# Optimization experiments

Measured on AMD Instinct MI355X. Metric: run time of the kernel, lower is better.

Reference implementation:

```python
import jax, jax.numpy as jnp
import numpy as np

B, S, H = 2, 1024, 4096
NH, DH, NKV = 32, 128, 2          # heads, head_dim, kv groups
ROT = DH // 2                      # 64: GLM rotates first half of head dim
GROUP = NH // NKV                  # 16 query heads per kv group
SCALE = DH ** -0.5


def glm_rope(x, pos):
    """GLM interleaved rotary on first ROT dims. x: [B,S,h,DH], pos: [B,S] int."""
    rot, rest = x[..., :ROT], x[..., ROT:]
    inv_freq = 1.0 / (10000.0 ** (jnp.arange(0, ROT, 2, dtype=jnp.float32) / ROT))  # [ROT/2]
    ang = pos.astype(jnp.float32)[:, :, None] * inv_freq[None, None, :]             # [B,S,ROT/2]
    cos = jnp.cos(ang)[:, :, None, :]
    sin = jnp.sin(ang)[:, :, None, :]
    x0, x1 = rot[..., 0::2], rot[..., 1::2]
    o0 = x0 * cos - x1 * sin
    o1 = x1 * cos + x0 * sin
    rot_out = jnp.stack([o0, o1], axis=-1).reshape(rot.shape)
    return jnp.concatenate([rot_out, rest], axis=-1)


def setup_inputs() -> dict:
    key = jax.random.key(0)
    k1, k2, k3, k4 = jax.random.split(key, 4)
    return {
        "hidden_states": jax.random.normal(k1, (B, S, H), jnp.float32) * 0.02,
        "position_ids": jnp.arange(B * S, dtype=jnp.int32).reshape(B, S) % S,
        "W_qkv": jax.random.normal(k2, (H, NH * DH + 2 * NKV * DH), jnp.float32) * 0.02,
        "b_qkv": jax.random.normal(k3, (NH * DH + 2 * NKV * DH,), jnp.float32) * 0.02,
        "W_dense": jax.random.normal(k4, (NH * DH, H), jnp.float32) * 0.02,
    }


def reference(hidden_states, position_ids, W_qkv, b_qkv, W_dense):
    qkv = hidden_states @ W_qkv + b_qkv                              # [B,S,4608]
    q = qkv[..., : NH * DH].reshape(B, S, NH, DH)
    k = qkv[..., NH * DH : NH * DH + NKV * DH].reshape(B, S, NKV, DH)
    v = qkv[..., NH * DH + NKV * DH :].reshape(B, S, NKV, DH)

    q = glm_rope(q, position_ids)
    k = glm_rope(k, position_ids)

    # GQA: expand kv groups to all heads
    k = jnp.repeat(k, GROUP, axis=2)                                 # [B,S,NH,DH]
    v = jnp.repeat(v, GROUP, axis=2)

    scores = jnp.einsum("bqhd,bkhd->bhqk", q, k) * SCALE             # [B,NH,S,S]
    causal = jnp.tril(jnp.ones((S, S), dtype=bool))
    scores = jnp.where(causal[None, None], scores, jnp.finfo(scores.dtype).min)
    probs = jax.nn.softmax(scores, axis=-1)
    ctx = jnp.einsum("bhqk,bkhd->bqhd", probs, v).reshape(B, S, NH * DH)
    return ctx @ W_dense                                             # [B,S,H]
```

## Files before the change

### kernel.cpp

```cpp
#include <hip/hip_runtime.h>

#define B_    2
#define S_    1024
#define H_    4096
#define NH_   32
#define DH_   128
#define NKV_  2
#define GROUP_ 16
#define ROT_  64
#define NQKV_ 4608
#define SCALE_ 0.08838834764831845f
#define KVB   64

typedef __attribute__((ext_vector_type(8))) short bf16x8;
typedef __attribute__((ext_vector_type(4))) float f32x4;

typedef __attribute__((address_space(1))) const void* gptr_t;
typedef __attribute__((address_space(3))) void* lptr_t;

__device__ __forceinline__ unsigned short f2bf(float f) {
    unsigned int u = __builtin_bit_cast(unsigned int, f);
    u += 0x7FFFu + ((u >> 16) & 1u);
    return (unsigned short)(u >> 16);
}
__device__ __forceinline__ unsigned int pack2bf(float a, float b) {
    return (unsigned int)f2bf(a) | ((unsigned int)f2bf(b) << 16);
}

__global__ void k_f32_to_bf16(const float* __restrict__ in,
                              unsigned short* __restrict__ out, int n4) {
    int i = blockIdx.x * blockDim.x + threadIdx.x;
    if (i >= n4) return;
    const float4 v = reinterpret_cast<const float4*>(in)[i];
    ushort4 o;
    o.x = f2bf(v.x); o.y = f2bf(v.y); o.z = f2bf(v.z); o.w = f2bf(v.w);
    reinterpret_cast<ushort4*>(out)[i] = o;
}

__global__ void k_transpose_bf16(const float* __restrict__ in,
                                 unsigned short* __restrict__ out,
                                 int K, int N) {
    __shared__ float tile[32][33];
    const int n0 = blockIdx.x * 32, k0 = blockIdx.y * 32;
    const int tx = threadIdx.x, ty = threadIdx.y;
    for (int j = ty; j < 32; j += 8)
        tile[j][tx] = in[(size_t)(k0 + j) * N + n0 + tx];
    __syncthreads();
    for (int j = ty; j < 32; j += 8)
        out[(size_t)(n0 + j) * K + k0 + tx] = f2bf(tile[tx][j]);
}

__global__ __launch_bounds__(256, 2) void k_gemm_bt(
    const unsigned short* __restrict__ A,
    const unsigned short* __restrict__ Bt,
    const float* __restrict__ bias,
    float* __restrict__ Cf,
    int M, int N, int K)
{
    __shared__ __align__(16) char lds[2][32768];

    const int tid  = threadIdx.x;
    const int wave = tid >> 6, lane = tid & 63;
    const int lrow = lane & 15, lhi = lane >> 4;
    const int wm = (wave >> 1) * 64, wn = (wave & 1) * 64;
    const size_t a_row0 = (size_t)blockIdx.y * 128;
    const size_t b_col0 = (size_t)blockIdx.x * 128;

    const size_t strideK = (size_t)K * 2;
    const char* Asrc = (const char*)A + (a_row0 + (tid >> 3)) * strideK;
    const char* Bsrc = (const char*)Bt + (b_col0 + (tid >> 3)) * strideK;
    const int swz_src = ((tid & 7) * 16) ^ (((tid >> 3) & 7) << 4);
    const int dst_off = tid * 16;

    f32x4 acc[4][4] = {};
    const int nt = K >> 6;

    #pragma unroll
    for (int j = 0; j < 4; j++) {
        __builtin_amdgcn_global_load_lds(
            (gptr_t)(Asrc + (size_t)j * 32 * strideK + swz_src),
            (lptr_t)(lds[0] + j * 4096 + dst_off), 16, 0, 0);
        __builtin_amdgcn_global_load_lds(
            (gptr_t)(Bsrc + (size_t)j * 32 * strideK + swz_src),
            (lptr_t)(lds[0] + 16384 + j * 4096 + dst_off), 16, 0, 0);
    }

    int cur = 0;
    for (int t = 0; t < nt; t++) {
        if (t + 1 < nt) {
            const size_t kb = (size_t)(t + 1) * 128;
            #pragma unroll
            for (int j = 0; j < 4; j++) {
                __builtin_amdgcn_global_load_lds(
                    (gptr_t)(Asrc + (size_t)j * 32 * strideK + kb + swz_src),
                    (lptr_t)(lds[cur ^ 1] + j * 4096 + dst_off), 16, 0, 0);
                __builtin_amdgcn_global_load_lds(
                    (gptr_t)(Bsrc + (size_t)j * 32 * strideK + kb + swz_src),
                    (lptr_t)(lds[cur ^ 1] + 16384 + j * 4096 + dst_off), 16, 0, 0);
            }
            asm volatile("s_waitcnt vmcnt(8)" ::: "memory");
        } else {
            asm volatile("s_waitcnt vmcnt(0)" ::: "memory");
        }
        __builtin_amdgcn_s_barrier();

        const char* La = lds[cur];
        const char* Lb = lds[cur] + 16384;
        bf16x8 af[4][2], bfr[4][2];
        #pragma unroll
        for (int i = 0; i < 4; i++) {
            const int fr = wm + i * 16 + lrow;
            af[i][0] = *(const bf16x8*)(La + fr * 128 + ((lhi * 16) ^ ((fr & 7) << 4)));
            af[i][1] = *(const bf16x8*)(La + fr * 128 + ((64 + lhi * 16) ^ ((fr & 7) << 4)));
        }
        #pragma unroll
        for (int j = 0; j < 4; j++) {
            const int br = wn + j * 16 + lrow;
            bfr[j][0] = *(const bf16x8*)(Lb + br * 128 + ((lhi * 16) ^ ((br & 7) << 4)));
            bfr[j][1] = *(const bf16x8*)(Lb + br * 128 + ((64 + lhi * 16) ^ ((br & 7) << 4)));
        }
        #pragma unroll
        for (int i = 0; i < 4; i++)
            #pragma unroll
            for (int j = 0; j < 4; j++) {
                acc[i][j] = __builtin_amdgcn_mfma_f32_16x16x32_bf16(
                    af[i][0], bfr[j][0], acc[i][j], 0, 0, 0);
                acc[i][j] = __builtin_amdgcn_mfma_f32_16x16x32_bf16(
                    af[i][1], bfr[j][1], acc[i][j], 0, 0, 0);
            }
        __builtin_amdgcn_s_barrier();
        cur ^= 1;
    }

    #pragma unroll
    for (int i = 0; i < 4; i++)
        #pragma unroll
        for (int j = 0; j < 4; j++) {
            const size_t grow0 = a_row0 + wm + i * 16 + lhi * 4;
            const size_t gcol  = b_col0 + wn + j * 16 + lrow;
            const float bi = bias ? bias[gcol] : 0.f;
            #pragma unroll
            for (int r = 0; r < 4; r++)
                Cf[(grow0 + r) * N + gcol] = acc[i][j][r] + bi;
        }
}

__global__ void k_rope_reorg(const float* __restrict__ qkv,
                             const int* __restrict__ pos_ids,
                             unsigned short* __restrict__ Qh,
                             unsigned short* __restrict__ Kh,
                             unsigned short* __restrict__ Vt)
{
    const int NPR = (NH_ + 2 * NKV_) * 64;
    const int idx = blockIdx.x * blockDim.x + threadIdx.x;
    if (idx >= B_ * S_ * NPR) return;
    const int t = idx / NPR;
    const int rem = idx % NPR;
    const int unit = rem >> 6;
    const int pr = rem & 63;
    const int b = t >> 10, s = t & 1023;
    const float pos = (float)pos_ids[t];
    const float* row = qkv + (size_t)t * NQKV_;

    if (unit < NH_) {
        const int col = unit * DH_ + 2 * pr;
        float x0 = row[col], x1 = row[col + 1];
        if (pr < 32) {
            const float ang = pos * powf(10000.f, -(float)pr / 32.f);
            float sn, cs; sincosf(ang, &sn, &cs);
            const float o0 = x0 * cs - x1 * sn;
            const float o1 = x1 * cs + x0 * sn;
            x0 = o0; x1 = o1;
        }
        unsigned short* dst = Qh + ((size_t)((b * NH_ + unit) * S_) + s) * DH_ + 2 * pr;
        dst[0] = f2bf(x0); dst[1] = f2bf(x1);
    } else if (unit < NH_ + NKV_) {
        const int g = unit - NH_;
        const int col = NH_ * DH_ + g * DH_ + 2 * pr;
        float x0 = row[col], x1 = row[col + 1];
        if (pr < 32) {
            const float ang = pos * powf(10000.f, -(float)pr / 32.f);
            float sn, cs; sincosf(ang, &sn, &cs);
            const float o0 = x0 * cs - x1 * sn;
            const float o1 = x1 * cs + x0 * sn;
            x0 = o0; x1 = o1;
        }
        unsigned short* dst = Kh + ((size_t)((b * NKV_ + g) * S_) + s) * DH_ + 2 * pr;
        dst[0] = f2bf(x0); dst[1] = f2bf(x1);
    } else {
        const int g = unit - NH_ - NKV_;
        const int col = NH_ * DH_ + NKV_ * DH_ + g * DH_ + 2 * pr;
        const float x0 = row[col], x1 = row[col + 1];
        unsigned short* d0 = Vt + ((size_t)((b * NKV_ + g) * DH_) + 2 * pr) * S_ + s;
        d0[0]  = f2bf(x0);
        d0[S_] = f2bf(x1);
    }
}

__global__ __launch_bounds__(256) void k_attn(
    const unsigned short* __restrict__ Qh,
    const unsigned short* __restrict__ Kh,
    const unsigned short* __restrict__ Vt,
    unsigned short* __restrict__ ctx)
{
    __shared__ __align__(16) char lds_kt[2][16384];
    __shared__ __align__(16) char lds_vt[16384];
    __shared__ __align__(16) char lds_p[4][2048];

    const int tid  = threadIdx.x;
    const int wave = tid >> 6, lane = tid & 63;
    const int lrow = lane & 15, lhi = lane >> 4;
    char* myp = lds_p[wave];

    const int blk  = blockIdx.x;
    const int pair = blk & 7;
    const int h    = (blk >> 3) & 31;
    const int b    = blk >> 8;
    const int g    = h >> 4;

    const char* Kbase = (const char*)(Kh + (size_t)((b * NKV_ + g) * S_) * DH_);
    const char* Vbase = (const char*)(Vt + (size_t)((b * NKV_ + g) * DH_) * S_);

    const int kcol = lrow * 16;
    const int vrow_l = lane >> 3;
    const int vcol = (lane & 7) * 16;

    for (int half = 0; half < 2; half++) {
        const int qt = half ? (15 - pair) : pair;
        const int q0 = qt * 64 + wave * 16;
        const int ntiles = qt + 1;
        const int q_glob = q0 + lrow;

        #pragma unroll
        for (int i = 0; i < 4; i++) {
            const int ci = wave * 4 + i;
            const int r  = ci * 4 + lhi;
            __builtin_amdgcn_global_load_lds(
                (gptr_t)(Kbase + (size_t)r * 256 + (kcol ^ ((r & 7) << 4))),
                (lptr_t)(lds_kt[0] + ci * 1024), 16, 0, 0);
        }
        const unsigned short* Qp = Qh + ((size_t)((b * NH_ + h) * S_) + q0) * DH_;
        bf16x8 a_q[4];
        #pragma unroll
        for (int ks = 0; ks < 4; ks++)
            a_q[ks] = *(const bf16x8*)(Qp + (size_t)lrow * DH_ + ks * 32 + lhi * 8);
        asm volatile("s_waitcnt vmcnt(0)" ::: "memory");
        __builtin_amdgcn_s_barrier();

        float m_run = -1e30f, l_run = 0.f;
        f32x4 o_acc[8] = {};
        int cur = 0;

        for (int t = 0; t < ntiles; t++) {
            const bool has_next = (t + 1 < ntiles);
            #pragma unroll
            for (int i = 0; i < 4; i++) {
                const int ci = wave * 4 + i;
                const int r  = ci * 8 + vrow_l;
                __builtin_amdgcn_global_load_lds(
                    (gptr_t)(Vbase + (size_t)r * (S_ * 2) + t * (KVB * 2)
                             + (vcol ^ ((r & 7) << 4))),
                    (lptr_t)(lds_vt + ci * 1024), 16, 0, 0);
            }
            if (has_next) {
                const char* ksrc = Kbase + (size_t)(t + 1) * 16384;
                #pragma unroll
                for (int i = 0; i < 4; i++) {
                    const int ci = wave * 4 + i;
                    const int r  = ci * 4 + lhi;
                    __builtin_amdgcn_global_load_lds(
                        (gptr_t)(ksrc + (size_t)r * 256 + (kcol ^ ((r & 7) << 4))),
                        (lptr_t)(lds_kt[cur ^ 1] + ci * 1024), 16, 0, 0);
                }
            }
            f32x4 s_acc[4] = {};
            #pragma unroll
            for (int sub = 0; sub < 4; sub++) {
                const int r = sub * 16 + lrow;
                #pragma unroll
                for (int ks = 0; ks < 4; ks++) {
                    const bf16x8 a_k = *(const bf16x8*)(
                        lds_kt[cur] + r * 256 + ((ks * 64 + lhi * 16) ^ ((r & 7) << 4)));
                    s_acc[sub] = __builtin_amdgcn_mfma_f32_16x16x32_bf16(
                        a_k, a_q[ks], s_acc[sub], 0, 0, 0);
                }
            }
            float pv[16];
            float mx = -1e30f;
            if (!has_next) {
                #pragma unroll
                for (int sub = 0; sub < 4; sub++)
                    #pragma unroll
                    for (int r = 0; r < 4; r++) {
                        const int kvg = t * KVB + sub * 16 + lhi * 4 + r;
                        float sv = s_acc[sub][r] * SCALE_;
                        if (kvg > q_glob) sv = -1e30f;
                        pv[sub * 4 + r] = sv;
                        mx = fmaxf(mx, sv);
                    }
            } else {
                #pragma unroll
                for (int sub = 0; sub < 4; sub++)
                    #pragma unroll
                    for (int r = 0; r < 4; r++) {
                        const float sv = s_acc[sub][r] * SCALE_;
                        pv[sub * 4 + r] = sv;
                        mx = fmaxf(mx, sv);
                    }
            }
            mx = fmaxf(mx, __shfl_xor(mx, 16));
            mx = fmaxf(mx, __shfl_xor(mx, 32));
            const float mnew = fmaxf(m_run, mx);
            const float scale = __expf(m_run - mnew);
            m_run = mnew;
            float sm = 0.f;
            #pragma unroll
            for (int i = 0; i < 16; i++) {
                const float e = __expf(pv[i] - mnew);
                pv[i] = e;
                sm += e;
            }
            sm += __shfl_xor(sm, 16);
            sm += __shfl_xor(sm, 32);
            l_run = l_run * scale + sm;
            #pragma unroll
            for (int d = 0; d < 8; d++) {
                o_acc[d][0] *= scale; o_acc[d][1] *= scale;
                o_acc[d][2] *= scale; o_acc[d][3] *= scale;
            }
            #pragma unroll
            for (int sub = 0; sub < 4; sub++) {
                const int off = (lrow * 128 + sub * 32 + lhi * 8) ^ ((lrow & 7) << 4);
                *reinterpret_cast<uint2*>(myp + off) = make_uint2(
                    pack2bf(pv[sub * 4 + 0], pv[sub * 4 + 1]),
                    pack2bf(pv[sub * 4 + 2], pv[sub * 4 + 3]));
            }
            bf16x8 a_p[2];
            #pragma unroll
            for (int frag = 0; frag < 2; frag++) {
                const int off = (lrow * 128 + frag * 64 + lhi * 16) ^ ((lrow & 7) << 4);
                a_p[frag] = *reinterpret_cast<const bf16x8*>(myp + off);
            }
            if (has_next) asm volatile("s_waitcnt vmcnt(4)" ::: "memory");
            else          asm volatile("s_waitcnt vmcnt(0)" ::: "memory");
            __builtin_amdgcn_s_barrier();
            #pragma unroll
            for (int d = 0; d < 8; d++) {
                const int r = d * 16 + lrow;
                #pragma unroll
                for (int frag = 0; frag < 2; frag++) {
                    const bf16x8 a_v = *(const bf16x8*)(
                        lds_vt + r * 128 + ((frag * 64 + lhi * 16) ^ ((r & 7) << 4)));
                    o_acc[d] = __builtin_amdgcn_mfma_f32_16x16x32_bf16(
                        a_v, a_p[frag], o_acc[d], 0, 0, 0);
                }
            }
            asm volatile("s_waitcnt vmcnt(0)" ::: "memory");
            __builtin_amdgcn_s_barrier();
            cur ^= 1;
        }
        const float inv = 1.f / l_run;
        const size_t row = (size_t)b * S_ + q0 + lrow;
        #pragma unroll
        for (int d = 0; d < 8; d++) {
            unsigned short* dst = ctx + row * (NH_ * DH_) + h * DH_ + d * 16 + lhi * 4;
            *reinterpret_cast<uint2*>(dst) = make_uint2(
                pack2bf(o_acc[d][0] * inv, o_acc[d][1] * inv),
                pack2bf(o_acc[d][2] * inv, o_acc[d][3] * inv));
        }
    }
}

extern "C" void kernel_launch(void* const* d_in, const int* in_sizes, int n_in,
                              void* d_out, int out_size, void* d_ws, size_t ws_size,
                              hipStream_t stream)
{
    const float* hidden  = (const float*)d_in[0];
    const int*   pos_ids = (const int*)d_in[1];
    const float* W_qkv   = (const float*)d_in[2];
    const float* b_qkv   = (const float*)d_in[3];
    const float* W_dense = (const float*)d_in[4];
    float* out = (float*)d_out;

    char* ws = (char*)d_ws;
    unsigned short* Xbf = (unsigned short*)(ws);
    unsigned short* Wqt = (unsigned short*)(ws + 16777216);
    unsigned short* Wdt = (unsigned short*)(ws + 54525952);
    float*          qkv = (float*)         (ws + 88080384);
    unsigned short* Qh  = (unsigned short*)(ws + 125829120);
    unsigned short* Kh  = (unsigned short*)(ws + 142606336);
    unsigned short* Vt  = (unsigned short*)(ws + 143654912);
    unsigned short* Ctx = (unsigned short*)(ws + 144703488);

    const int M = B_ * S_;

    k_f32_to_bf16<<<(M * H_ / 4 + 255) / 256, 256, 0, stream>>>(hidden, Xbf, M * H_ / 4);
    dim3 tb(32, 8);
    k_transpose_bf16<<<dim3(NQKV_ / 32, H_ / 32), tb, 0, stream>>>(W_qkv, Wqt, H_, NQKV_);
    k_transpose_bf16<<<dim3(H_ / 32, H_ / 32), tb, 0, stream>>>(W_dense, Wdt, H_, H_);
    k_gemm_bt<<<dim3(NQKV_ / 128, M / 128), 256, 0, stream>>>(
        Xbf, Wqt, b_qkv, qkv, M, NQKV_, H_);
    k_rope_reorg<<<(M * 2304 + 255) / 256, 256, 0, stream>>>(qkv, pos_ids, Qh, Kh, Vt);
    k_attn<<<B_ * NH_ * 8, 256, 0, stream>>>(Qh, Kh, Vt, Ctx);
    k_gemm_bt<<<dim3(H_ / 128, M / 128), 256, 0, stream>>>(
        Ctx, Wdt, nullptr, out, M, H_, H_);
}
```

Baseline: 305.8 us.

## Fuse RoPE and head reorganization into QKV GEMM epilogue; switch to 32x32 MFMA

Folds the rotary embedding, bias add and scatter into Q/K/Vt bf16 layouts into the QKV GEMM epilogue through a MODE template. This removes the fp32 qkv intermediate write and read and one kernel launch. Both GEMMs also move from 16x16x32 to 32x32x16 bf16 MFMA tiles with a new fragment loading order. The trade-off is heavier epilogue work in the GEMM (sincos per element, scattered 2-byte stores) and different register use.

```diff
diff --git a/kernel.cpp b/kernel.cpp
--- a/kernel.cpp
+++ b/kernel.cpp
@@ -14,6 +14,7 @@
 
 typedef __attribute__((ext_vector_type(8))) short bf16x8;
 typedef __attribute__((ext_vector_type(4))) float f32x4;
+typedef __attribute__((ext_vector_type(16))) float f32x16;
 
 typedef __attribute__((address_space(1))) const void* gptr_t;
 typedef __attribute__((address_space(3))) void* lptr_t;
@@ -50,18 +51,23 @@
         out[(size_t)(n0 + j) * K + k0 + tx] = f2bf(tile[tx][j]);
 }
 
-__global__ __launch_bounds__(256, 2) void k_gemm_bt(
+template<int MODE>
+__global__ __launch_bounds__(256, 2) void k_gemm(
     const unsigned short* __restrict__ A,
     const unsigned short* __restrict__ Bt,
     const float* __restrict__ bias,
     float* __restrict__ Cf,
+    const int* __restrict__ pos_ids,
+    unsigned short* __restrict__ Qh,
+    unsigned short* __restrict__ Kh,
+    unsigned short* __restrict__ Vt,
     int M, int N, int K)
 {
     __shared__ __align__(16) char lds[2][32768];
 
     const int tid  = threadIdx.x;
     const int wave = tid >> 6, lane = tid & 63;
-    const int lrow = lane & 15, lhi = lane >> 4;
+    const int l31 = lane & 31, l1 = lane >> 5;
     const int wm = (wave >> 1) * 64, wn = (wave & 1) * 64;
     const size_t a_row0 = (size_t)blockIdx.y * 128;
     const size_t b_col0 = (size_t)blockIdx.x * 128;
@@ -72,7 +78,7 @@
     const int swz_src = ((tid & 7) * 16) ^ (((tid >> 3) & 7) << 4);
     const int dst_off = tid * 16;
 
-    f32x4 acc[4][4] = {};
+    f32x16 acc[2][2] = {};
     const int nt = K >> 6;
 
     #pragma unroll
@@ -106,95 +112,90 @@
 
         const char* La = lds[cur];
         const char* Lb = lds[cur] + 16384;
-        bf16x8 af[4][2], bfr[4][2];
         #pragma unroll
-        for (int i = 0; i < 4; i++) {
-            const int fr = wm + i * 16 + lrow;
-            af[i][0] = *(const bf16x8*)(La + fr * 128 + ((lhi * 16) ^ ((fr & 7) << 4)));
-            af[i][1] = *(const bf16x8*)(La + fr * 128 + ((64 + lhi * 16) ^ ((fr & 7) << 4)));
-        }
-        #pragma unroll
-        for (int j = 0; j < 4; j++) {
-            const int br = wn + j * 16 + lrow;
-            bfr[j][0] = *(const bf16x8*)(Lb + br * 128 + ((lhi * 16) ^ ((br & 7) << 4)));
-            bfr[j][1] = *(const bf16x8*)(Lb + br * 128 + ((64 + lhi * 16) ^ ((br & 7) << 4)));
-        }
-        #pragma unroll
-        for (int i = 0; i < 4; i++)
-            #pragma unroll
-            for (int j = 0; j < 4; j++) {
-                acc[i][j] = __builtin_amdgcn_mfma_f32_16x16x32_bf16(
-                    af[i][0], bfr[j][0], acc[i][j], 0, 0, 0);
-                acc[i][j] = __builtin_amdgcn_mfma_f32_16x16x32_bf16(
-                    af[i][1], bfr[j][1], acc[i][j], 0, 0, 0);
-            }
+        for (int kc = 0; kc < 4; kc++) {
+            const int cb = kc * 32 + l1 * 16;
+            bf16x8 af[2], bfr[2];
+            #pragma unroll
+            for (int mi = 0; mi < 2; mi++) {
+                const int r = wm + mi * 32 + l31;
+                af[mi] = *(const bf16x8*)(La + r * 128 + (cb ^ ((r & 7) << 4)));
+            }
+            #pragma unroll
+            for (int ni = 0; ni < 2; ni++) {
+                const int r = wn + ni * 32 + l31;
+                bfr[ni] = *(const bf16x8*)(Lb + r * 128 + (cb ^ ((r & 7) << 4)));
+            }
+            #pragma unroll
+            for (int mi = 0; mi < 2; mi++)
+                #pragma unroll
+                for (int ni = 0; ni < 2; ni++)
+                    acc[mi][ni] = __builtin_amdgcn_mfma_f32_32x32x16_bf16(
+                        af[mi], bfr[ni], acc[mi][ni], 0, 0, 0);
+        }
         __builtin_amdgcn_s_barrier();
         cur ^= 1;
     }
 
     #pragma unroll
-    for (int i = 0; i < 4; i++)
+    for (int mi = 0; mi < 2; mi++)
         #pragma unroll
-        for (int j = 0; j < 4; j++) {
-            const size_t grow0 = a_row0 + wm + i * 16 + lhi * 4;
-            const size_t gcol  = b_col0 + wn + j * 16 + lrow;
-            const float bi = bias ? bias[gcol] : 0.f;
-            #pragma unroll
-            for (int r = 0; r < 4; r++)
-                Cf[(grow0 + r) * N + gcol] = acc[i][j][r] + bi;
-        }
-}
-
-__global__ void k_rope_reorg(const float* __restrict__ qkv,
-                             const int* __restrict__ pos_ids,
-                             unsigned short* __restrict__ Qh,
-                             unsigned short* __restrict__ Kh,
-                             unsigned short* __restrict__ Vt)
-{
-    const int NPR = (NH_ + 2 * NKV_) * 64;
-    const int idx = blockIdx.x * blockDim.x + threadIdx.x;
-    if (idx >= B_ * S_ * NPR) return;
-    const int t = idx / NPR;
-    const int rem = idx % NPR;
-    const int unit = rem >> 6;
-    const int pr = rem & 63;
-    const int b = t >> 10, s = t & 1023;
-    const float pos = (float)pos_ids[t];
-    const float* row = qkv + (size_t)t * NQKV_;
-
-    if (unit < NH_) {
-        const int col = unit * DH_ + 2 * pr;
-        float x0 = row[col], x1 = row[col + 1];
-        if (pr < 32) {
-            const float ang = pos * powf(10000.f, -(float)pr / 32.f);
-            float sn, cs; sincosf(ang, &sn, &cs);
-            const float o0 = x0 * cs - x1 * sn;
-            const float o1 = x1 * cs + x0 * sn;
-            x0 = o0; x1 = o1;
-        }
-        unsigned short* dst = Qh + ((size_t)((b * NH_ + unit) * S_) + s) * DH_ + 2 * pr;
-        dst[0] = f2bf(x0); dst[1] = f2bf(x1);
-    } else if (unit < NH_ + NKV_) {
-        const int g = unit - NH_;
-        const int col = NH_ * DH_ + g * DH_ + 2 * pr;
-        float x0 = row[col], x1 = row[col + 1];
-        if (pr < 32) {
-            const float ang = pos * powf(10000.f, -(float)pr / 32.f);
-            float sn, cs; sincosf(ang, &sn, &cs);
-            const float o0 = x0 * cs - x1 * sn;
-            const float o1 = x1 * cs + x0 * sn;
-            x0 = o0; x1 = o1;
-        }
-        unsigned short* dst = Kh + ((size_t)((b * NKV_ + g) * S_) + s) * DH_ + 2 * pr;
-        dst[0] = f2bf(x0); dst[1] = f2bf(x1);
-    } else {
-        const int g = unit - NH_ - NKV_;
-        const int col = NH_ * DH_ + NKV_ * DH_ + g * DH_ + 2 * pr;
-        const float x0 = row[col], x1 = row[col + 1];
-        unsigned short* d0 = Vt + ((size_t)((b * NKV_ + g) * DH_) + 2 * pr) * S_ + s;
-        d0[0]  = f2bf(x0);
-        d0[S_] = f2bf(x1);
-    }
+        for (int ni = 0; ni < 2; ni++) {
+            const int dloc = wn + ni * 32 + l31;
+            const size_t colg = b_col0 + dloc;
+            const float bi = (MODE == 1 || bias) ? bias[colg] : 0.f;
+            float v[16];
+            #pragma unroll
+            for (int r = 0; r < 16; r++) v[r] = acc[mi][ni][r] + bi;
+            const size_t row0 = a_row0 + wm + mi * 32 + 4 * l1;
+
+            if (MODE == 0) {
+                #pragma unroll
+                for (int r = 0; r < 16; r++) {
+                    const size_t row = row0 + (r & 3) + 8 * (r >> 2);
+                    Cf[row * N + colg] = v[r];
+                }
+            } else {
+                const int bx = (int)blockIdx.x;
+                const size_t bb = row0 >> 10;
+                if (bx < 34) {
+                    if (dloc < 64) {
+                        const int pr = dloc >> 1;
+                        const float freq = powf(10000.f, -(float)pr / 32.f);
+                        #pragma unroll
+                        for (int r = 0; r < 16; r++) {
+                            const size_t row = row0 + (r & 3) + 8 * (r >> 2);
+                            const float pos = (float)pos_ids[row];
+                            float sn, cs; sincosf(pos * freq, &sn, &cs);
+                            const float partner = __shfl_xor(v[r], 1);
+                            v[r] = (dloc & 1) ? (v[r] * cs + partner * sn)
+                                              : (v[r] * cs - partner * sn);
+                        }
+                    }
+                    unsigned short* dst;
+                    if (bx < 32)
+                        dst = Qh + ((bb * NH_ + bx) * S_) * DH_ + dloc;
+                    else
+                        dst = Kh + ((bb * NKV_ + (bx - 32)) * S_) * DH_ + dloc;
+                    #pragma unroll
+                    for (int r = 0; r < 16; r++) {
+                        const size_t row = row0 + (r & 3) + 8 * (r >> 2);
+                        dst[(row & 1023) * DH_] = f2bf(v[r]);
+                    }
+                } else {
+                    const int g = bx - 34;
+                    unsigned short* dst =
+                        Vt + ((bb * NKV_ + g) * DH_ + dloc) * S_;
+                    #pragma unroll
+                    for (int q = 0; q < 4; q++) {
+                        const size_t s = (row0 + 8 * q) & 1023;
+                        *reinterpret_cast<uint2*>(dst + s) = make_uint2(
+                            pack2bf(v[q * 4 + 0], v[q * 4 + 1]),
+                            pack2bf(v[q * 4 + 2], v[q * 4 + 3]));
+                    }
+                }
+            }
+        }
 }
 
 __global__ __launch_bounds__(256) void k_attn(
@@ -386,7 +387,6 @@
     unsigned short* Xbf = (unsigned short*)(ws);
     unsigned short* Wqt = (unsigned short*)(ws + 16777216);
     unsigned short* Wdt = (unsigned short*)(ws + 54525952);
-    float*          qkv = (float*)         (ws + 88080384);
     unsigned short* Qh  = (unsigned short*)(ws + 125829120);
     unsigned short* Kh  = (unsigned short*)(ws + 142606336);
     unsigned short* Vt  = (unsigned short*)(ws + 143654912);
@@ -398,10 +398,9 @@
     dim3 tb(32, 8);
     k_transpose_bf16<<<dim3(NQKV_ / 32, H_ / 32), tb, 0, stream>>>(W_qkv, Wqt, H_, NQKV_);
     k_transpose_bf16<<<dim3(H_ / 32, H_ / 32), tb, 0, stream>>>(W_dense, Wdt, H_, H_);
-    k_gemm_bt<<<dim3(NQKV_ / 128, M / 128), 256, 0, stream>>>(
-        Xbf, Wqt, b_qkv, qkv, M, NQKV_, H_);
-    k_rope_reorg<<<(M * 2304 + 255) / 256, 256, 0, stream>>>(qkv, pos_ids, Qh, Kh, Vt);
+    k_gemm<1><<<dim3(NQKV_ / 128, M / 128), 256, 0, stream>>>(
+        Xbf, Wqt, b_qkv, nullptr, pos_ids, Qh, Kh, Vt, M, NQKV_, H_);
     k_attn<<<B_ * NH_ * 8, 256, 0, stream>>>(Qh, Kh, Vt, Ctx);
-    k_gemm_bt<<<dim3(H_ / 128, M / 128), 256, 0, stream>>>(
-        Ctx, Wdt, nullptr, out, M, H_, H_);
-}
+    k_gemm<0><<<dim3(H_ / 128, M / 128), 256, 0, stream>>>(
+        Ctx, Wdt, nullptr, out, nullptr, nullptr, nullptr, nullptr, M, H_, H_);
+}
```

Measured after the change: 327.2 us. +7.0%, slower.
